# Kernel tuning notes

Hardware: AMD Instinct MI355X
Metric: run time of the kernel (lower is better)

## Reference

```python
import jax, jax.numpy as jnp
import numpy as np

B = 65536
EPS = 1e-5


def _cnot(psi, c, t):
    # psi: [B,2,2,2,2]; qubit q lives on axis q+1. CNOT flips target where control=1.
    c_ax, t_ax = c + 1, t + 1
    p0 = jax.lax.index_in_dim(psi, 0, c_ax, keepdims=True)
    p1 = jax.lax.index_in_dim(psi, 1, c_ax, keepdims=True)
    p1 = jnp.flip(p1, axis=t_ax)
    return jnp.concatenate([p0, p1], axis=c_ax)


def setup_inputs() -> dict:
    key = jax.random.key(0)
    x = jax.random.normal(key, (B, 1, 28, 28), dtype=jnp.float32)
    gamma = jnp.ones((4,), jnp.float32)   # BatchNorm1d(4) weight
    beta = jnp.zeros((4,), jnp.float32)   # BatchNorm1d(4) bias
    return {"x": x, "gamma": gamma, "beta": beta}


def reference(x, gamma, beta):
    bsz = x.shape[0]
    # avg_pool2d(x, 6): kernel=stride=6, no padding -> uses only the top-left 24x24
    pooled = x[:, :, :24, :24].reshape(bsz, 1, 4, 6, 4, 6).mean(axis=(3, 5))
    pooled = pooled.reshape(bsz, 16)
    theta = pooled[:, ::4]  # x[:, i*4] for i=0..3 -> [B,4] RY angles
    half = 0.5 * theta
    q = jnp.stack([jnp.cos(half), jnp.sin(half)], axis=-1)  # [B,4,2], RY|0> amplitudes (real)
    psi = jnp.einsum('bi,bj,bk,bl->bijkl', q[:, 0], q[:, 1], q[:, 2], q[:, 3])
    for c, t in ((0, 1), (1, 2), (2, 3), (3, 0)):
        psi = _cnot(psi, c, t)
    probs = psi * psi  # amplitudes are real
    signs = jnp.array([1.0, -1.0], jnp.float32)
    # <Z_i> = sum_s probs[s] * (-1)^{s_i}
    zs = [jnp.tensordot(probs, signs, axes=[[i + 1], [0]]).sum(axis=(1, 2, 3))
          for i in range(4)]
    out = jnp.stack(zs, axis=1)  # [B,4]
    # BatchNorm1d(4), training mode (biased batch variance)
    mean = out.mean(axis=0)
    var = out.var(axis=0)
    return gamma * (out - mean) / jnp.sqrt(var + EPS) + beta
```

## Files before the change

### kernel.cpp

```cpp
#include <hip/hip_runtime.h>

#define EPS 1e-5f


__global__ __launch_bounds__(256) void qnat_k1(const float* __restrict__ x,
                                               float* __restrict__ z_out,
                                               float* __restrict__ partials,
                                               int bsz) {
    const int t    = threadIdx.x;
    const int lane = t & 63;
    const int w    = t >> 6;
    const int img0 = blockIdx.x * 16 + w * 4;

    const bool b0 = (lane & 1) != 0;
    const bool b1 = (lane & 2) != 0;
    const int  k  = lane & 3;

    const int j1 = 64 + lane, j2 = 128 + lane;
    const int m0 = lane % 7, p0 = lane / 42;
    const int m1 = j1 % 7,   p1 = j1 / 42;
    const int m2 = j2 % 7,   p2 = j2 / 42;

    float s1 = 0.f, s2 = 0.f;

    #pragma unroll
    for (int pr = 0; pr < 2; ++pr) {
        const int imgA = img0 + pr * 2;
        const int imgB = imgA + 1;

        float4 vA0 = make_float4(0.f,0.f,0.f,0.f), vA1 = vA0, vA2 = vA0;
        float4 vB0 = vA0, vB1 = vA0, vB2 = vA0;
        if (imgA < bsz) {
            const float* ipA = x + (size_t)imgA * 784;
            vA0 = *reinterpret_cast<const float4*>(ipA + 4 * lane);
            vA1 = *reinterpret_cast<const float4*>(ipA + 4 * j1);
            if (lane < 40) vA2 = *reinterpret_cast<const float4*>(ipA + 4 * j2);
        }
        if (imgB < bsz) {
            const float* ipB = x + (size_t)imgB * 784;
            vB0 = *reinterpret_cast<const float4*>(ipB + 4 * lane);
            vB1 = *reinterpret_cast<const float4*>(ipB + 4 * j1);
            if (lane < 40) vB2 = *reinterpret_cast<const float4*>(ipB + 4 * j2);
        }

        float aA0 = 0.f, aA1 = 0.f, aA2 = 0.f, aA3 = 0.f;
        float aB0 = 0.f, aB1 = 0.f, aB2 = 0.f, aB3 = 0.f;
        {
            float h2 = vA0.x + vA0.y, h4 = h2 + vA0.z + vA0.w;
            float c  = (m0 == 0) ? h4 : ((m0 == 1) ? h2 : 0.f);
            aA0 += (p0 == 0) ? c : 0.f; aA1 += (p0 == 1) ? c : 0.f;
            aA2 += (p0 == 2) ? c : 0.f; aA3 += (p0 == 3) ? c : 0.f;
            h2 = vB0.x + vB0.y; h4 = h2 + vB0.z + vB0.w;
            c  = (m0 == 0) ? h4 : ((m0 == 1) ? h2 : 0.f);
            aB0 += (p0 == 0) ? c : 0.f; aB1 += (p0 == 1) ? c : 0.f;
            aB2 += (p0 == 2) ? c : 0.f; aB3 += (p0 == 3) ? c : 0.f;

            h2 = vA1.x + vA1.y; h4 = h2 + vA1.z + vA1.w;
            c  = (m1 == 0) ? h4 : ((m1 == 1) ? h2 : 0.f);
            aA0 += (p1 == 0) ? c : 0.f; aA1 += (p1 == 1) ? c : 0.f;
            aA2 += (p1 == 2) ? c : 0.f; aA3 += (p1 == 3) ? c : 0.f;
            h2 = vB1.x + vB1.y; h4 = h2 + vB1.z + vB1.w;
            c  = (m1 == 0) ? h4 : ((m1 == 1) ? h2 : 0.f);
            aB0 += (p1 == 0) ? c : 0.f; aB1 += (p1 == 1) ? c : 0.f;
            aB2 += (p1 == 2) ? c : 0.f; aB3 += (p1 == 3) ? c : 0.f;

            h2 = vA2.x + vA2.y; h4 = h2 + vA2.z + vA2.w;
            c  = (m2 == 0) ? h4 : ((m2 == 1) ? h2 : 0.f);
            aA0 += (p2 == 0) ? c : 0.f; aA1 += (p2 == 1) ? c : 0.f;
            aA2 += (p2 == 2) ? c : 0.f; aA3 += (p2 == 3) ? c : 0.f;
            h2 = vB2.x + vB2.y; h4 = h2 + vB2.z + vB2.w;
            c  = (m2 == 0) ? h4 : ((m2 == 1) ? h2 : 0.f);
            aB0 += (p2 == 0) ? c : 0.f; aB1 += (p2 == 1) ? c : 0.f;
            aB2 += (p2 == 2) ? c : 0.f; aB3 += (p2 == 3) ? c : 0.f;
        }

        float rA = __shfl_xor(b0 ? aA0 : aA1, 1, 64);
        float rB = __shfl_xor(b0 ? aB0 : aB1, 1, 64);
        float uA = (b0 ? aA1 : aA0) + rA;
        float uB = (b0 ? aB1 : aB0) + rB;
        rA = __shfl_xor(b0 ? aA2 : aA3, 1, 64);
        rB = __shfl_xor(b0 ? aB2 : aB3, 1, 64);
        float vA = (b0 ? aA3 : aA2) + rA;
        float vB = (b0 ? aB3 : aB2) + rB;
        rA = __shfl_xor(b1 ? uA : vA, 2, 64);
        rB = __shfl_xor(b1 ? uB : vB, 2, 64);
        float wA = (b1 ? vA : uA) + rA;
        float wB = (b1 ? vB : uB) + rB;
        #pragma unroll
        for (int off = 4; off < 64; off <<= 1) {
            wA += __shfl_xor(wA, off, 64);
            wB += __shfl_xor(wB, off, 64);
        }

        const float kk = 1.0f / 36.0f;
        const float cA = __cosf(wA * kk);
        const float cB = __cosf(wB * kk);
        const float cm1A = __shfl_xor(cA, 1, 64);
        const float cm1B = __shfl_xor(cB, 1, 64);
        const float cm2A = __shfl_xor(cA, 2, 64);
        const float cm2B = __shfl_xor(cB, 2, 64);
        const float cm3A = __shfl_xor(cm2A, 1, 64);
        const float cm3B = __shfl_xor(cm2B, 1, 64);

        const float t3A = cm2A * cm3A, fullA = cm1A * t3A;
        const float t3B = cm2B * cm3B, fullB = cm1B * t3B;
        const float zA = (k == 0) ? fullA : (k == 1) ? cA * cm1A
                       : (k == 2) ? cA * t3A : cA * fullA;
        const float zB = (k == 0) ? fullB : (k == 1) ? cB * cm1B
                       : (k == 2) ? cB * t3B : cB * fullB;

        if (lane < 8) {
            const int  im = (lane < 4) ? imgA : imgB;
            const float zz = (lane < 4) ? zA : zB;
            if (im < bsz) z_out[(size_t)im * 4 + k] = zz;
        }
        const float zAm = (imgA < bsz) ? zA : 0.f;
        const float zBm = (imgB < bsz) ? zB : 0.f;
        s1 += zAm + zBm;
        s2 += zAm * zAm + zBm * zBm;
    }

    __shared__ float ps[4][8];
    if (lane < 4) { ps[w][lane] = s1; ps[w][4 + lane] = s2; }
    __syncthreads();
    if (t < 8) {
        partials[blockIdx.x * 8 + t] = (ps[0][t] + ps[1][t]) + (ps[2][t] + ps[3][t]);
    }
}

__global__ __launch_bounds__(256) void qnat_k2(const float* __restrict__ z,
                                               const float* __restrict__ partials,
                                               const float* __restrict__ gamma,
                                               const float* __restrict__ beta,
                                               float* __restrict__ out,
                                               int NB, int bsz) {
    __shared__ float red[4][8];
    __shared__ float st[8];

    const int t = threadIdx.x, lane = t & 63, w = t >> 6;

    float acc[8] = {0.f,0.f,0.f,0.f,0.f,0.f,0.f,0.f};
    for (int r = t; r < NB; r += 256) {
        const float4 a = *reinterpret_cast<const float4*>(partials + r * 8);
        const float4 b = *reinterpret_cast<const float4*>(partials + r * 8 + 4);
        acc[0] += a.x; acc[1] += a.y; acc[2] += a.z; acc[3] += a.w;
        acc[4] += b.x; acc[5] += b.y; acc[6] += b.z; acc[7] += b.w;
    }
    #pragma unroll
    for (int off = 1; off < 64; off <<= 1) {
        #pragma unroll
        for (int kk = 0; kk < 8; ++kk) acc[kk] += __shfl_xor(acc[kk], off, 64);
    }
    if (lane == 0) {
        #pragma unroll
        for (int kk = 0; kk < 8; ++kk) red[w][kk] = acc[kk];
    }
    __syncthreads();
    if (t < 8) st[t] = (red[0][t] + red[1][t]) + (red[2][t] + red[3][t]);
    __syncthreads();
    if (t < 4) {
        const double invB = 1.0 / (double)bsz;
        const double m   = (double)st[t] * invB;
        const double var = (double)st[4 + t] * invB - m * m;
        st[t]     = (float)m;
        st[4 + t] = gamma[t] * rsqrtf((float)var + EPS);
    }
    __syncthreads();

    const int img0 = blockIdx.x * 1024 + t;
    #pragma unroll
    for (int i = 0; i < 4; ++i) {
        const int img = img0 + i * 256;
        if (img < bsz) {
            const float4 zv = reinterpret_cast<const float4*>(z)[img];
            float4 o;
            o.x = (zv.x - st[0]) * st[4] + beta[0];
            o.y = (zv.y - st[1]) * st[5] + beta[1];
            o.z = (zv.z - st[2]) * st[6] + beta[2];
            o.w = (zv.w - st[3]) * st[7] + beta[3];
            reinterpret_cast<float4*>(out)[img] = o;
        }
    }
}

extern "C" void kernel_launch(void* const* d_in, const int* in_sizes, int n_in,
                              void* d_out, int out_size, void* d_ws, size_t ws_size,
                              hipStream_t stream) {
    const float* x     = (const float*)d_in[0];
    const float* gamma = (const float*)d_in[1];
    const float* beta  = (const float*)d_in[2];
    float* out = (float*)d_out;

    const int bsz = in_sizes[0] / 784;
    const int NB  = (bsz + 15) / 16;
    const int NB2 = (bsz + 1023) / 1024;

    float* z        = (float*)d_ws;
    float* partials = (float*)((char*)d_ws + (size_t)bsz * 16);

    qnat_k1<<<NB, 256, 0, stream>>>(x, z, partials, bsz);
    qnat_k2<<<NB2, 256, 0, stream>>>(z, partials, gamma, beta, out, NB, bsz);
}
```

Baseline: 39.40 us.

## Fuse pooling/quantum stage and BatchNorm into one cooperative persistent kernel

Replaces the two-kernel pipeline with a single cooperative kernel sized to full occupancy. Each block processes several images, keeps their z values in shared memory, writes per-block partial sums, performs a grid-wide sync, then every block reduces the partials and normalizes its own images. This removes the second launch and the global round trip of z, at the cost of a grid barrier, redundant partial reductions in every block, and per-call host occupancy queries. The original two-kernel path remains as a fallback if the cooperative launch fails.

Measured after the change: 131.4 us. +233.6%, slower.

```diff
diff --git a/kernel.cpp b/kernel.cpp
--- a/kernel.cpp
+++ b/kernel.cpp
@@ -1,6 +1,193 @@
 #include <hip/hip_runtime.h>
+#include <hip/hip_cooperative_groups.h>
+
+namespace cg = cooperative_groups;
 
 #define EPS 1e-5f
+#define TPB 256
+
+
+__device__ __forceinline__ void qnat_pair(const float* __restrict__ x, int bsz,
+                                          int imgA, int imgB, int lane,
+                                          int j1, int j2, int m0, int p0, int m1, int p1,
+                                          int m2, int p2, bool b0, bool b1, int k,
+                                          float& zA, float& zB) {
+    float4 vA0 = make_float4(0.f,0.f,0.f,0.f), vA1 = vA0, vA2 = vA0;
+    float4 vB0 = vA0, vB1 = vA0, vB2 = vA0;
+    if (imgA < bsz) {
+        const float* ipA = x + (size_t)imgA * 784;
+        vA0 = *reinterpret_cast<const float4*>(ipA + 4 * lane);
+        vA1 = *reinterpret_cast<const float4*>(ipA + 4 * j1);
+        if (lane < 40) vA2 = *reinterpret_cast<const float4*>(ipA + 4 * j2);
+    }
+    if (imgB < bsz) {
+        const float* ipB = x + (size_t)imgB * 784;
+        vB0 = *reinterpret_cast<const float4*>(ipB + 4 * lane);
+        vB1 = *reinterpret_cast<const float4*>(ipB + 4 * j1);
+        if (lane < 40) vB2 = *reinterpret_cast<const float4*>(ipB + 4 * j2);
+    }
+
+    float aA0 = 0.f, aA1 = 0.f, aA2 = 0.f, aA3 = 0.f;
+    float aB0 = 0.f, aB1 = 0.f, aB2 = 0.f, aB3 = 0.f;
+    {
+        float h2 = vA0.x + vA0.y, h4 = h2 + vA0.z + vA0.w;
+        float c  = (m0 == 0) ? h4 : ((m0 == 1) ? h2 : 0.f);
+        aA0 += (p0 == 0) ? c : 0.f; aA1 += (p0 == 1) ? c : 0.f;
+        aA2 += (p0 == 2) ? c : 0.f; aA3 += (p0 == 3) ? c : 0.f;
+        h2 = vB0.x + vB0.y; h4 = h2 + vB0.z + vB0.w;
+        c  = (m0 == 0) ? h4 : ((m0 == 1) ? h2 : 0.f);
+        aB0 += (p0 == 0) ? c : 0.f; aB1 += (p0 == 1) ? c : 0.f;
+        aB2 += (p0 == 2) ? c : 0.f; aB3 += (p0 == 3) ? c : 0.f;
+
+        h2 = vA1.x + vA1.y; h4 = h2 + vA1.z + vA1.w;
+        c  = (m1 == 0) ? h4 : ((m1 == 1) ? h2 : 0.f);
+        aA0 += (p1 == 0) ? c : 0.f; aA1 += (p1 == 1) ? c : 0.f;
+        aA2 += (p1 == 2) ? c : 0.f; aA3 += (p1 == 3) ? c : 0.f;
+        h2 = vB1.x + vB1.y; h4 = h2 + vB1.z + vB1.w;
+        c  = (m1 == 0) ? h4 : ((m1 == 1) ? h2 : 0.f);
+        aB0 += (p1 == 0) ? c : 0.f; aB1 += (p1 == 1) ? c : 0.f;
+        aB2 += (p1 == 2) ? c : 0.f; aB3 += (p1 == 3) ? c : 0.f;
+
+        h2 = vA2.x + vA2.y; h4 = h2 + vA2.z + vA2.w;
+        c  = (m2 == 0) ? h4 : ((m2 == 1) ? h2 : 0.f);
+        aA0 += (p2 == 0) ? c : 0.f; aA1 += (p2 == 1) ? c : 0.f;
+        aA2 += (p2 == 2) ? c : 0.f; aA3 += (p2 == 3) ? c : 0.f;
+        h2 = vB2.x + vB2.y; h4 = h2 + vB2.z + vB2.w;
+        c  = (m2 == 0) ? h4 : ((m2 == 1) ? h2 : 0.f);
+        aB0 += (p2 == 0) ? c : 0.f; aB1 += (p2 == 1) ? c : 0.f;
+        aB2 += (p2 == 2) ? c : 0.f; aB3 += (p2 == 3) ? c : 0.f;
+    }
+
+    float rA = __shfl_xor(b0 ? aA0 : aA1, 1, 64);
+    float rB = __shfl_xor(b0 ? aB0 : aB1, 1, 64);
+    float uA = (b0 ? aA1 : aA0) + rA;
+    float uB = (b0 ? aB1 : aB0) + rB;
+    rA = __shfl_xor(b0 ? aA2 : aA3, 1, 64);
+    rB = __shfl_xor(b0 ? aB2 : aB3, 1, 64);
+    float vA = (b0 ? aA3 : aA2) + rA;
+    float vB = (b0 ? aB3 : aB2) + rB;
+    rA = __shfl_xor(b1 ? uA : vA, 2, 64);
+    rB = __shfl_xor(b1 ? uB : vB, 2, 64);
+    float wA = (b1 ? vA : uA) + rA;
+    float wB = (b1 ? vB : uB) + rB;
+    #pragma unroll
+    for (int off = 4; off < 64; off <<= 1) {
+        wA += __shfl_xor(wA, off, 64);
+        wB += __shfl_xor(wB, off, 64);
+    }
+
+    const float kk = 1.0f / 36.0f;
+    const float cA = __cosf(wA * kk);
+    const float cB = __cosf(wB * kk);
+    const float cm1A = __shfl_xor(cA, 1, 64);
+    const float cm1B = __shfl_xor(cB, 1, 64);
+    const float cm2A = __shfl_xor(cA, 2, 64);
+    const float cm2B = __shfl_xor(cB, 2, 64);
+    const float cm3A = __shfl_xor(cm2A, 1, 64);
+    const float cm3B = __shfl_xor(cm2B, 1, 64);
+
+    const float t3A = cm2A * cm3A, fullA = cm1A * t3A;
+    const float t3B = cm2B * cm3B, fullB = cm1B * t3B;
+    zA = (k == 0) ? fullA : (k == 1) ? cA * cm1A : (k == 2) ? cA * t3A : cA * fullA;
+    zB = (k == 0) ? fullB : (k == 1) ? cB * cm1B : (k == 2) ? cB * t3B : cB * fullB;
+}
+
+__global__ __launch_bounds__(TPB, 4) void qnat_all(const float* __restrict__ x,
+                                                   const float* __restrict__ gamma,
+                                                   const float* __restrict__ beta,
+                                                   float* __restrict__ out,
+                                                   float* __restrict__ partials,
+                                                   int bsz, int ipb, int nblk) {
+    __shared__ float zsh[256][4];
+    __shared__ float ps[4][8];
+    __shared__ float red[4][8];
+    __shared__ float st[8];
+
+    const int t    = threadIdx.x;
+    const int lane = t & 63;
+    const int w    = t >> 6;
+    const int ipw  = ipb >> 2;
+    const int blk0 = blockIdx.x * ipb;
+    const int wimg0 = blk0 + w * ipw;
+
+    const bool b0 = (lane & 1) != 0;
+    const bool b1 = (lane & 2) != 0;
+    const int  k  = lane & 3;
+    const int j1 = 64 + lane, j2 = 128 + lane;
+    const int m0 = lane % 7, p0 = lane / 42;
+    const int m1 = j1 % 7,   p1 = j1 / 42;
+    const int m2 = j2 % 7,   p2 = j2 / 42;
+
+    float s1 = 0.f, s2 = 0.f;
+
+    for (int pr = 0; pr < (ipw >> 1); ++pr) {
+        const int imgA = wimg0 + pr * 2;
+        const int imgB = imgA + 1;
+        float zA, zB;
+        qnat_pair(x, bsz, imgA, imgB, lane, j1, j2, m0, p0, m1, p1, m2, p2, b0, b1, k, zA, zB);
+
+        if (lane < 8) {
+            const int im = (lane < 4) ? imgA : imgB;
+            const float zz = (lane < 4) ? zA : zB;
+            if (im < bsz) zsh[im - blk0][k] = zz;
+        }
+        const float zAm = (imgA < bsz) ? zA : 0.f;
+        const float zBm = (imgB < bsz) ? zB : 0.f;
+        s1 += zAm + zBm;
+        s2 += zAm * zAm + zBm * zBm;
+    }
+
+    if (lane < 4) { ps[w][lane] = s1; ps[w][4 + lane] = s2; }
+    __syncthreads();
+    if (t < 8) {
+        partials[blockIdx.x * 8 + t] = (ps[0][t] + ps[1][t]) + (ps[2][t] + ps[3][t]);
+    }
+
+    cg::this_grid().sync();
+
+    {
+        float acc[8] = {0.f,0.f,0.f,0.f,0.f,0.f,0.f,0.f};
+        for (int r = t; r < nblk; r += TPB) {
+            const float4 a = *reinterpret_cast<const float4*>(partials + r * 8);
+            const float4 b = *reinterpret_cast<const float4*>(partials + r * 8 + 4);
+            acc[0] += a.x; acc[1] += a.y; acc[2] += a.z; acc[3] += a.w;
+            acc[4] += b.x; acc[5] += b.y; acc[6] += b.z; acc[7] += b.w;
+        }
+        #pragma unroll
+        for (int off = 1; off < 64; off <<= 1) {
+            #pragma unroll
+            for (int kk = 0; kk < 8; ++kk) acc[kk] += __shfl_xor(acc[kk], off, 64);
+        }
+        if (lane == 0) {
+            #pragma unroll
+            for (int kk = 0; kk < 8; ++kk) red[w][kk] = acc[kk];
+        }
+        __syncthreads();
+        if (t < 8) st[t] = (red[0][t] + red[1][t]) + (red[2][t] + red[3][t]);
+        __syncthreads();
+        if (t < 4) {
+            const double invB = 1.0 / (double)bsz;
+            const double m   = (double)st[t] * invB;
+            const double var = (double)st[4 + t] * invB - m * m;
+            st[t]     = (float)m;
+            st[4 + t] = gamma[t] * rsqrtf((float)var + EPS);
+        }
+        __syncthreads();
+    }
+
+    for (int i = t; i < ipb; i += TPB) {
+        const int img = blk0 + i;
+        if (img < bsz) {
+            const float4 zv = *reinterpret_cast<const float4*>(&zsh[i][0]);
+            float4 o;
+            o.x = (zv.x - st[0]) * st[4] + beta[0];
+            o.y = (zv.y - st[1]) * st[5] + beta[1];
+            o.z = (zv.z - st[2]) * st[6] + beta[2];
+            o.w = (zv.w - st[3]) * st[7] + beta[3];
+            *reinterpret_cast<float4*>(out + (size_t)img * 4) = o;
+        }
+    }
+}
 
 
 __global__ __launch_bounds__(256) void qnat_k1(const float* __restrict__ x,
@@ -15,7 +202,6 @@
     const bool b0 = (lane & 1) != 0;
     const bool b1 = (lane & 2) != 0;
     const int  k  = lane & 3;
-
     const int j1 = 64 + lane, j2 = 128 + lane;
     const int m0 = lane % 7, p0 = lane / 42;
     const int m1 = j1 % 7,   p1 = j1 / 42;
@@ -27,90 +213,11 @@
     for (int pr = 0; pr < 2; ++pr) {
         const int imgA = img0 + pr * 2;
         const int imgB = imgA + 1;
-
-        float4 vA0 = make_float4(0.f,0.f,0.f,0.f), vA1 = vA0, vA2 = vA0;
-        float4 vB0 = vA0, vB1 = vA0, vB2 = vA0;
-        if (imgA < bsz) {
-            const float* ipA = x + (size_t)imgA * 784;
-            vA0 = *reinterpret_cast<const float4*>(ipA + 4 * lane);
-            vA1 = *reinterpret_cast<const float4*>(ipA + 4 * j1);
-            if (lane < 40) vA2 = *reinterpret_cast<const float4*>(ipA + 4 * j2);
-        }
-        if (imgB < bsz) {
-            const float* ipB = x + (size_t)imgB * 784;
-            vB0 = *reinterpret_cast<const float4*>(ipB + 4 * lane);
-            vB1 = *reinterpret_cast<const float4*>(ipB + 4 * j1);
-            if (lane < 40) vB2 = *reinterpret_cast<const float4*>(ipB + 4 * j2);
-        }
-
-        float aA0 = 0.f, aA1 = 0.f, aA2 = 0.f, aA3 = 0.f;
-        float aB0 = 0.f, aB1 = 0.f, aB2 = 0.f, aB3 = 0.f;
-        {
-            float h2 = vA0.x + vA0.y, h4 = h2 + vA0.z + vA0.w;
-            float c  = (m0 == 0) ? h4 : ((m0 == 1) ? h2 : 0.f);
-            aA0 += (p0 == 0) ? c : 0.f; aA1 += (p0 == 1) ? c : 0.f;
-            aA2 += (p0 == 2) ? c : 0.f; aA3 += (p0 == 3) ? c : 0.f;
-            h2 = vB0.x + vB0.y; h4 = h2 + vB0.z + vB0.w;
-            c  = (m0 == 0) ? h4 : ((m0 == 1) ? h2 : 0.f);
-            aB0 += (p0 == 0) ? c : 0.f; aB1 += (p0 == 1) ? c : 0.f;
-            aB2 += (p0 == 2) ? c : 0.f; aB3 += (p0 == 3) ? c : 0.f;
-
-            h2 = vA1.x + vA1.y; h4 = h2 + vA1.z + vA1.w;
-            c  = (m1 == 0) ? h4 : ((m1 == 1) ? h2 : 0.f);
-            aA0 += (p1 == 0) ? c : 0.f; aA1 += (p1 == 1) ? c : 0.f;
-            aA2 += (p1 == 2) ? c : 0.f; aA3 += (p1 == 3) ? c : 0.f;
-            h2 = vB1.x + vB1.y; h4 = h2 + vB1.z + vB1.w;
-            c  = (m1 == 0) ? h4 : ((m1 == 1) ? h2 : 0.f);
-            aB0 += (p1 == 0) ? c : 0.f; aB1 += (p1 == 1) ? c : 0.f;
-            aB2 += (p1 == 2) ? c : 0.f; aB3 += (p1 == 3) ? c : 0.f;
-
-            h2 = vA2.x + vA2.y; h4 = h2 + vA2.z + vA2.w;
-            c  = (m2 == 0) ? h4 : ((m2 == 1) ? h2 : 0.f);
-            aA0 += (p2 == 0) ? c : 0.f; aA1 += (p2 == 1) ? c : 0.f;
-            aA2 += (p2 == 2) ? c : 0.f; aA3 += (p2 == 3) ? c : 0.f;
-            h2 = vB2.x + vB2.y; h4 = h2 + vB2.z + vB2.w;
-            c  = (m2 == 0) ? h4 : ((m2 == 1) ? h2 : 0.f);
-            aB0 += (p2 == 0) ? c : 0.f; aB1 += (p2 == 1) ? c : 0.f;
-            aB2 += (p2 == 2) ? c : 0.f; aB3 += (p2 == 3) ? c : 0.f;
-        }
-
-        float rA = __shfl_xor(b0 ? aA0 : aA1, 1, 64);
-        float rB = __shfl_xor(b0 ? aB0 : aB1, 1, 64);
-        float uA = (b0 ? aA1 : aA0) + rA;
-        float uB = (b0 ? aB1 : aB0) + rB;
-        rA = __shfl_xor(b0 ? aA2 : aA3, 1, 64);
-        rB = __shfl_xor(b0 ? aB2 : aB3, 1, 64);
-        float vA = (b0 ? aA3 : aA2) + rA;
-        float vB = (b0 ? aB3 : aB2) + rB;
-        rA = __shfl_xor(b1 ? uA : vA, 2, 64);
-        rB = __shfl_xor(b1 ? uB : vB, 2, 64);
-        float wA = (b1 ? vA : uA) + rA;
-        float wB = (b1 ? vB : uB) + rB;
-        #pragma unroll
-        for (int off = 4; off < 64; off <<= 1) {
-            wA += __shfl_xor(wA, off, 64);
-            wB += __shfl_xor(wB, off, 64);
-        }
-
-        const float kk = 1.0f / 36.0f;
-        const float cA = __cosf(wA * kk);
-        const float cB = __cosf(wB * kk);
-        const float cm1A = __shfl_xor(cA, 1, 64);
-        const float cm1B = __shfl_xor(cB, 1, 64);
-        const float cm2A = __shfl_xor(cA, 2, 64);
-        const float cm2B = __shfl_xor(cB, 2, 64);
-        const float cm3A = __shfl_xor(cm2A, 1, 64);
-        const float cm3B = __shfl_xor(cm2B, 1, 64);
-
-        const float t3A = cm2A * cm3A, fullA = cm1A * t3A;
-        const float t3B = cm2B * cm3B, fullB = cm1B * t3B;
-        const float zA = (k == 0) ? fullA : (k == 1) ? cA * cm1A
-                       : (k == 2) ? cA * t3A : cA * fullA;
-        const float zB = (k == 0) ? fullB : (k == 1) ? cB * cm1B
-                       : (k == 2) ? cB * t3B : cB * fullB;
+        float zA, zB;
+        qnat_pair(x, bsz, imgA, imgB, lane, j1, j2, m0, p0, m1, p1, m2, p2, b0, b1, k, zA, zB);
 
         if (lane < 8) {
-            const int  im = (lane < 4) ? imgA : imgB;
+            const int im = (lane < 4) ? imgA : imgB;
             const float zz = (lane < 4) ? zA : zB;
             if (im < bsz) z_out[(size_t)im * 4 + k] = zz;
         }
@@ -136,7 +243,6 @@
                                                int NB, int bsz) {
     __shared__ float red[4][8];
     __shared__ float st[8];
-
     const int t = threadIdx.x, lane = t & 63, w = t >> 6;
 
     float acc[8] = {0.f,0.f,0.f,0.f,0.f,0.f,0.f,0.f};
@@ -192,12 +298,39 @@
     float* out = (float*)d_out;
 
     const int bsz = in_sizes[0] / 784;
-    const int NB  = (bsz + 15) / 16;
-    const int NB2 = (bsz + 1023) / 1024;
-
-    float* z        = (float*)d_ws;
-    float* partials = (float*)((char*)d_ws + (size_t)bsz * 16);
-
-    qnat_k1<<<NB, 256, 0, stream>>>(x, z, partials, bsz);
-    qnat_k2<<<NB2, 256, 0, stream>>>(z, partials, gamma, beta, out, NB, bsz);
-}
+
+    int numCU = 0, maxB = 0;
+    int dev = 0;
+    (void)hipGetDevice(&dev);
+    (void)hipDeviceGetAttribute(&numCU, hipDeviceAttributeMultiprocessorCount, dev);
+    (void)hipOccupancyMaxActiveBlocksPerMultiprocessor(&maxB, (const void*)qnat_all, TPB, 0);
+
+    bool launched = false;
+    if (numCU > 0 && maxB > 0) {
+        const int maxGrid = maxB * numCU;
+        int ipb = (bsz + maxGrid - 1) / maxGrid;
+        ipb = (ipb + 7) & ~7;
+        if (ipb <= 256) {
+            int grid = (bsz + ipb - 1) / ipb;
+            if (grid <= maxGrid) {
+                float* partials = (float*)d_ws;
+                int nblk = grid;
+                void* args[] = { (void*)&x, (void*)&gamma, (void*)&beta, (void*)&out,
+                                 (void*)&partials, (void*)&bsz, (void*)&ipb, (void*)&nblk };
+                hipError_t e = hipLaunchCooperativeKernel((const void*)qnat_all,
+                                                          dim3(grid), dim3(TPB),
+                                                          args, 0, stream);
+                launched = (e == hipSuccess);
+            }
+        }
+    }
+
+    if (!launched) {
+        const int NB  = (bsz + 15) / 16;
+        const int NB2 = (bsz + 1023) / 1024;
+        float* z        = (float*)d_ws;
+        float* partials = (float*)((char*)d_ws + (size_t)bsz * 16);
+        qnat_k1<<<NB, 256, 0, stream>>>(x, z, partials, bsz);
+        qnat_k2<<<NB2, 256, 0, stream>>>(z, partials, gamma, beta, out, NB, bsz);
+    }
+}
```
